# Kernel tuning notes

Measured on AMD Instinct MI355X. Metric: run time of the kernel, lower is better.

The kernel has to match this reference:

```python
import jax, jax.numpy as jnp
import numpy as np


def setup_inputs() -> dict:
    key = jax.random.key(0)
    k1, k2 = jax.random.split(key)
    B, N, C = 16, 8192, 256
    feat_points = jax.random.normal(k1, (B, N, C), dtype=jnp.float32)
    points = jax.random.uniform(k2, (B, N, 3), dtype=jnp.float32)  # coords in [0,1)
    return {"feat_points": feat_points, "points": points, "W": 32, "H": 32, "D": 32}


def reference(feat_points, points, W, H, D):
    # feat_points: [B, N, C], points: [B, N, 3] in [0,1)^3
    B, N, C = feat_points.shape
    WHD = W * H * D
    dims = jnp.array([W, H, D], dtype=jnp.float32)
    # voxel indices per point, clamped to grid bounds
    ijk = jnp.clip(jnp.floor(points * dims).astype(jnp.int32), 0,
                   jnp.array([W - 1, H - 1, D - 1], dtype=jnp.int32))  # [B,N,3]
    cell = ijk[..., 0] * (H * D) + ijk[..., 1] * D + ijk[..., 2]  # [B,N]
    # flatten batch into segment ids so one segment_max covers all batches
    seg = (cell + jnp.arange(B, dtype=jnp.int32)[:, None] * WHD).reshape(-1)  # [B*N]
    pooled = jax.ops.segment_max(feat_points.reshape(B * N, C), seg,
                                 num_segments=B * WHD)  # [B*WHD, C], -inf where empty
    # CUDA kernel initializes cells to 0 and scatter-maxes => max(0, per-cell max)
    out = jnp.maximum(pooled, 0.0).reshape(B, WHD, C)
    return jnp.transpose(out, (0, 2, 1)).reshape(B, C, W, H, D)
```

## Files before the change

kernel.cpp:

```cpp
#include <hip/hip_runtime.h>


#define CELLS_PER_BLK 512
#define CH_PER_BLK    16

typedef float float4v __attribute__((ext_vector_type(4)));
typedef int   int4v   __attribute__((ext_vector_type(4)));

__global__ __launch_bounds__(256) void k_count(
    const float* __restrict__ pts, int* __restrict__ cellId,
    int* __restrict__ counts, int BN, int N, int HD, int Dd, int WHD,
    float fW, float fH, float fD, int Wm1, int Hm1, int Dm1)
{
    int i = blockIdx.x * 256 + threadIdx.x;
    if (i >= BN) return;
    float x = pts[3 * i + 0];
    float y = pts[3 * i + 1];
    float z = pts[3 * i + 2];
    int ix = (int)floorf(x * fW); ix = ix < 0 ? 0 : (ix > Wm1 ? Wm1 : ix);
    int iy = (int)floorf(y * fH); iy = iy < 0 ? 0 : (iy > Hm1 ? Hm1 : iy);
    int iz = (int)floorf(z * fD); iz = iz < 0 ? 0 : (iz > Dm1 ? Dm1 : iz);
    int b = i / N;
    int seg = b * WHD + ix * HD + iy * Dd + iz;
    cellId[i] = seg;
    atomicAdd(&counts[seg], 1);
}

__global__ __launch_bounds__(256) void k_scan1(
    const int* __restrict__ counts, int* __restrict__ excl,
    int* __restrict__ blockSums, int n)
{
    __shared__ int lds[256];
    int tid = threadIdx.x;
    int i = blockIdx.x * 256 + tid;
    int v = (i < n) ? counts[i] : 0;
    lds[tid] = v;
    __syncthreads();
    for (int off = 1; off < 256; off <<= 1) {
        int t = (tid >= off) ? lds[tid - off] : 0;
        __syncthreads();
        lds[tid] += t;
        __syncthreads();
    }
    int incl = lds[tid];
    if (i < n) excl[i] = incl - v;
    if (tid == 255) blockSums[blockIdx.x] = incl;
}

__global__ __launch_bounds__(256) void k_scan2(int* __restrict__ blockSums, int nb)
{
    __shared__ int lds[256];
    __shared__ int carryS;
    int tid = threadIdx.x;
    if (tid == 0) carryS = 0;
    __syncthreads();
    int nChunks = (nb + 255) / 256;
    for (int ch = 0; ch < nChunks; ++ch) {
        int i = ch * 256 + tid;
        int v = (i < nb) ? blockSums[i] : 0;
        lds[tid] = v;
        __syncthreads();
        for (int off = 1; off < 256; off <<= 1) {
            int t = (tid >= off) ? lds[tid - off] : 0;
            __syncthreads();
            lds[tid] += t;
            __syncthreads();
        }
        int incl = lds[tid];
        int base = carryS;
        __syncthreads();
        if (i < nb) blockSums[i] = base + incl - v;
        if (tid == 255) carryS = base + incl;
        __syncthreads();
    }
}

__global__ __launch_bounds__(256) void k_scan3(
    int* __restrict__ excl, const int* __restrict__ blockSums,
    int* __restrict__ cur, int n, int total)
{
    int i = blockIdx.x * 256 + threadIdx.x;
    if (i < n) {
        int o = excl[i] + blockSums[blockIdx.x];
        excl[i] = o;
        cur[i] = o;
    }
    if (i == 0) excl[n] = total;
}

__global__ __launch_bounds__(256) void k_scatter(
    const int* __restrict__ cellId, int* __restrict__ cur,
    int2* __restrict__ ptCell, int BN)
{
    int i = blockIdx.x * 256 + threadIdx.x;
    if (i >= BN) return;
    int seg = cellId[i];
    int pos = atomicAdd(&cur[seg], 1);
    ptCell[pos] = make_int2(i, seg);
}

__global__ __launch_bounds__(256, 5) void k_pool(
    const float* __restrict__ feat, const int* __restrict__ offsets,
    const int2* __restrict__ ptCell, float* __restrict__ out,
    int C, int WHD, int nCb, int nChunk)
{
    __shared__ int lds[CH_PER_BLK * CELLS_PER_BLK];

    int lin = blockIdx.x;
    int nwg = gridDim.x;
    int swz = (lin & 7) * (nwg >> 3) + (lin >> 3);
    int cb    = swz % nCb;
    int rest  = swz / nCb;
    int chunk = rest % nChunk;
    int b     = rest / nChunk;

    int segBase = b * WHD + cb * CELLS_PER_BLK;
    int c0 = chunk * CH_PER_BLK;

    int4v* l4 = reinterpret_cast<int4v*>(lds);
    int4v zero = {0, 0, 0, 0};
#pragma unroll
    for (int it = 0; it < (CH_PER_BLK * CELLS_PER_BLK / 4) / 256; ++it)
        l4[threadIdx.x + 256 * it] = zero;
    __syncthreads();

    int p0 = offsets[segBase];
    int p1 = offsets[segBase + CELLS_PER_BLK];
    int tSub  = threadIdx.x >> 4;
    int cLane = threadIdx.x & 15;
    const float* fbase = feat + c0 + cLane;

    for (int pb = p0 + tSub; pb < p1; pb += 64) {
        int2  pc[4];
        float v[4];
#pragma unroll
        for (int k = 0; k < 4; ++k) {
            int p  = pb + 16 * k;
            int pp = p < p1 ? p : p1 - 1;
            pc[k] = ptCell[pp];
        }
#pragma unroll
        for (int k = 0; k < 4; ++k)
            v[k] = fbase[(size_t)pc[k].x * C];
#pragma unroll
        for (int k = 0; k < 4; ++k) {
            if (pb + 16 * k < p1) {
                int cell = pc[k].y - segBase;
                int addr = cLane * CELLS_PER_BLK + (cell ^ (cLane << 2));
                atomicMax(&lds[addr], __float_as_int(fmaxf(v[k], 0.0f)));
            }
        }
    }
    __syncthreads();

    const float* ldsF = reinterpret_cast<const float*>(lds);
#pragma unroll
    for (int it = 0; it < (CH_PER_BLK * CELLS_PER_BLK / 4) / 256; ++it) {
        int f = threadIdx.x + 256 * it;
        int c = f >> 7;
        int q = f & 127;
        int base = c * CELLS_PER_BLK + ((q * 4) ^ (c << 2));
        float4v v = *reinterpret_cast<const float4v*>(ldsF + base);
        size_t ob = ((size_t)(b * C + c0 + c)) * (size_t)WHD
                  + (size_t)cb * CELLS_PER_BLK + q * 4;
        __builtin_nontemporal_store(v, reinterpret_cast<float4v*>(out + ob));
    }
}

extern "C" void kernel_launch(void* const* d_in, const int* in_sizes, int n_in,
                              void* d_out, int out_size, void* d_ws, size_t ws_size,
                              hipStream_t stream)
{
    const float* feat = (const float*)d_in[0];
    const float* pts  = (const float*)d_in[1];

    int BN  = in_sizes[1] / 3;
    int C   = in_sizes[0] / BN;
    const int W = 32, H = 32, Dd = 32;
    int WHD = W * H * Dd;
    int B   = out_size / (C * WHD);
    int N   = BN / B;
    int NSEG = B * WHD;
    int nBlocksScan = (NSEG + 255) / 256;

    char* w = (char*)d_ws;
    auto alloc = [&](size_t bytes) -> void* {
        void* p = (void*)w;
        w += ((bytes + 255) / 256) * 256;
        return p;
    };
    int*  cellId    = (int*)alloc((size_t)BN * 4);
    int*  counts    = (int*)alloc((size_t)NSEG * 4);
    int*  offsets   = (int*)alloc(((size_t)NSEG + 1) * 4);
    int*  cur       = (int*)alloc((size_t)NSEG * 4);
    int*  blockSums = (int*)alloc((size_t)nBlocksScan * 4);
    int2* ptCell    = (int2*)alloc((size_t)BN * 8);
    (void)ws_size;

    hipMemsetAsync(counts, 0, (size_t)NSEG * 4, stream);

    k_count<<<(BN + 255) / 256, 256, 0, stream>>>(
        pts, cellId, counts, BN, N, H * Dd, Dd, WHD,
        (float)W, (float)H, (float)Dd, W - 1, H - 1, Dd - 1);

    k_scan1<<<nBlocksScan, 256, 0, stream>>>(counts, offsets, blockSums, NSEG);
    k_scan2<<<1, 256, 0, stream>>>(blockSums, nBlocksScan);
    k_scan3<<<nBlocksScan, 256, 0, stream>>>(offsets, blockSums, cur, NSEG, BN);

    k_scatter<<<(BN + 255) / 256, 256, 0, stream>>>(cellId, cur, ptCell, BN);

    int nCb = WHD / CELLS_PER_BLK;
    int nChunk = C / CH_PER_BLK;
    int nwg = nCb * nChunk * B;
    k_pool<<<nwg, 256, 0, stream>>>(feat, offsets, ptCell,
                                    (float*)d_out, C, WHD, nCb, nChunk);
}
```

Before: 139.8 us.

## Bucket points by 512-cell pool block instead of per cell, single-block scan

Counting sort now bins points by coarse pool-block index rather than exact voxel cell. The prefix sum shrinks to 1024 entries and runs as one block, replacing the three-kernel multi-pass scan and reducing the memset size. In exchange, the atomic counters in the count and scatter kernels see much higher contention, since many points share each coarse bin.

```diff
diff --git a/kernel.cpp b/kernel.cpp
--- a/kernel.cpp
+++ b/kernel.cpp
@@ -23,69 +23,30 @@
     int b = i / N;
     int seg = b * WHD + ix * HD + iy * Dd + iz;
     cellId[i] = seg;
-    atomicAdd(&counts[seg], 1);
+    atomicAdd(&counts[seg >> 9], 1);
 }
 
-__global__ __launch_bounds__(256) void k_scan1(
-    const int* __restrict__ counts, int* __restrict__ excl,
-    int* __restrict__ blockSums, int n)
+__global__ __launch_bounds__(1024) void k_scan(
+    const int* __restrict__ counts, int* __restrict__ offsets,
+    int* __restrict__ cur, int n, int total)
 {
-    __shared__ int lds[256];
+    __shared__ int lds[1024];
     int tid = threadIdx.x;
-    int i = blockIdx.x * 256 + tid;
-    int v = (i < n) ? counts[i] : 0;
+    int v = (tid < n) ? counts[tid] : 0;
     lds[tid] = v;
     __syncthreads();
-    for (int off = 1; off < 256; off <<= 1) {
+    for (int off = 1; off < 1024; off <<= 1) {
         int t = (tid >= off) ? lds[tid - off] : 0;
         __syncthreads();
         lds[tid] += t;
         __syncthreads();
     }
-    int incl = lds[tid];
-    if (i < n) excl[i] = incl - v;
-    if (tid == 255) blockSums[blockIdx.x] = incl;
-}
-
-__global__ __launch_bounds__(256) void k_scan2(int* __restrict__ blockSums, int nb)
-{
-    __shared__ int lds[256];
-    __shared__ int carryS;
-    int tid = threadIdx.x;
-    if (tid == 0) carryS = 0;
-    __syncthreads();
-    int nChunks = (nb + 255) / 256;
-    for (int ch = 0; ch < nChunks; ++ch) {
-        int i = ch * 256 + tid;
-        int v = (i < nb) ? blockSums[i] : 0;
-        lds[tid] = v;
-        __syncthreads();
-        for (int off = 1; off < 256; off <<= 1) {
-            int t = (tid >= off) ? lds[tid - off] : 0;
-            __syncthreads();
-            lds[tid] += t;
-            __syncthreads();
-        }
-        int incl = lds[tid];
-        int base = carryS;
-        __syncthreads();
-        if (i < nb) blockSums[i] = base + incl - v;
-        if (tid == 255) carryS = base + incl;
-        __syncthreads();
+    if (tid < n) {
+        int e = lds[tid] - v;
+        offsets[tid] = e;
+        cur[tid] = e;
     }
-}
-
-__global__ __launch_bounds__(256) void k_scan3(
-    int* __restrict__ excl, const int* __restrict__ blockSums,
-    int* __restrict__ cur, int n, int total)
-{
-    int i = blockIdx.x * 256 + threadIdx.x;
-    if (i < n) {
-        int o = excl[i] + blockSums[blockIdx.x];
-        excl[i] = o;
-        cur[i] = o;
-    }
-    if (i == 0) excl[n] = total;
+    if (tid == 0) offsets[n] = total;
 }
 
 __global__ __launch_bounds__(256) void k_scatter(
@@ -95,7 +56,7 @@
     int i = blockIdx.x * 256 + threadIdx.x;
     if (i >= BN) return;
     int seg = cellId[i];
-    int pos = atomicAdd(&cur[seg], 1);
+    int pos = atomicAdd(&cur[seg >> 9], 1);
     ptCell[pos] = make_int2(i, seg);
 }
 
@@ -124,8 +85,9 @@
         l4[threadIdx.x + 256 * it] = zero;
     __syncthreads();
 
-    int p0 = offsets[segBase];
-    int p1 = offsets[segBase + CELLS_PER_BLK];
+    int coarse = b * nCb + cb;
+    int p0 = offsets[coarse];
+    int p1 = offsets[coarse + 1];
     int tSub  = threadIdx.x >> 4;
     int cLane = threadIdx.x & 15;
     const float* fbase = feat + c0 + cLane;
@@ -180,8 +142,8 @@
     int WHD = W * H * Dd;
     int B   = out_size / (C * WHD);
     int N   = BN / B;
-    int NSEG = B * WHD;
-    int nBlocksScan = (NSEG + 255) / 256;
+    int nCb = WHD / CELLS_PER_BLK;
+    int NSEGC = B * nCb;
 
     char* w = (char*)d_ws;
     auto alloc = [&](size_t bytes) -> void* {
@@ -189,27 +151,23 @@
         w += ((bytes + 255) / 256) * 256;
         return p;
     };
-    int*  cellId    = (int*)alloc((size_t)BN * 4);
-    int*  counts    = (int*)alloc((size_t)NSEG * 4);
-    int*  offsets   = (int*)alloc(((size_t)NSEG + 1) * 4);
-    int*  cur       = (int*)alloc((size_t)NSEG * 4);
-    int*  blockSums = (int*)alloc((size_t)nBlocksScan * 4);
-    int2* ptCell    = (int2*)alloc((size_t)BN * 8);
+    int*  cellId  = (int*)alloc((size_t)BN * 4);
+    int*  counts  = (int*)alloc((size_t)NSEGC * 4);
+    int*  offsets = (int*)alloc(((size_t)NSEGC + 1) * 4);
+    int*  cur     = (int*)alloc((size_t)NSEGC * 4);
+    int2* ptCell  = (int2*)alloc((size_t)BN * 8);
     (void)ws_size;
 
-    hipMemsetAsync(counts, 0, (size_t)NSEG * 4, stream);
+    hipMemsetAsync(counts, 0, (size_t)NSEGC * 4, stream);
 
     k_count<<<(BN + 255) / 256, 256, 0, stream>>>(
         pts, cellId, counts, BN, N, H * Dd, Dd, WHD,
         (float)W, (float)H, (float)Dd, W - 1, H - 1, Dd - 1);
 
-    k_scan1<<<nBlocksScan, 256, 0, stream>>>(counts, offsets, blockSums, NSEG);
-    k_scan2<<<1, 256, 0, stream>>>(blockSums, nBlocksScan);
-    k_scan3<<<nBlocksScan, 256, 0, stream>>>(offsets, blockSums, cur, NSEG, BN);
+    k_scan<<<1, 1024, 0, stream>>>(counts, offsets, cur, NSEGC, BN);
 
     k_scatter<<<(BN + 255) / 256, 256, 0, stream>>>(cellId, cur, ptCell, BN);
 
-    int nCb = WHD / CELLS_PER_BLK;
     int nChunk = C / CH_PER_BLK;
     int nwg = nCb * nChunk * B;
     k_pool<<<nwg, 256, 0, stream>>>(feat, offsets, ptCell,
```

New measurement: 145.8 us. 4.3% more time.
